# Kernel optimization log

Hardware: AMD Instinct MI355X
Metric: run time of the kernel (lower is better)

Reference implementation:

```python
import jax, jax.numpy as jnp
import numpy as np

B, N, E = 4, 20000, 320000          # batch, billboards, edges
F_NODE, F_AD = 16, 8                # raw feature dims
H, L, HEADS = 64, 2, 4              # hidden, message-passing layers, attn heads


def layer_norm(x, g, b, eps=1e-5):
    mu = x.mean(-1, keepdims=True)
    var = ((x - mu) ** 2).mean(-1, keepdims=True)
    return (x - mu) / jnp.sqrt(var + eps) * g + b


def setup_inputs() -> dict:
    key = jax.random.key(0)
    ks = jax.random.split(key, 16)
    s = lambda i, shape, sc: jax.random.normal(ks[i], shape, jnp.float32) * sc
    return {
        'graph_nodes': s(0, (B, N, F_NODE), 1.0),
        'current_ad': s(1, (B, F_AD), 1.0),
        'w_node': s(2, (F_NODE, H), 0.1), 'b_node': jnp.zeros((H,), jnp.float32),
        'msg_w': s(3, (L, 2 * H, H), 0.05), 'msg_b': jnp.zeros((L, H), jnp.float32),
        'upd_w': s(4, (L, 2 * H, H), 0.05), 'upd_b': jnp.zeros((L, H), jnp.float32),
        'w_ad': s(5, (F_AD, H), 0.1), 'b_ad': jnp.zeros((H,), jnp.float32),
        'wq': s(6, (H, H), 0.1), 'bq': jnp.zeros((H,), jnp.float32),
        'wk': s(7, (H, H), 0.1), 'bk': jnp.zeros((H,), jnp.float32),
        'wv': s(8, (H, H), 0.1), 'bv': jnp.zeros((H,), jnp.float32),
        'wo': s(9, (H, H), 0.1), 'bo': jnp.zeros((H,), jnp.float32),
        'ln_g': jnp.ones((H,), jnp.float32), 'ln_b': jnp.zeros((H,), jnp.float32),
        'policy_w': s(10, (H,), 0.1), 'policy_b': jnp.zeros((), jnp.float32),
        'graph_edge_links': jax.random.randint(ks[11], (B, 2, E), 0, N),
        'mask': jax.random.randint(ks[12], (B, N), 0, 2).astype(bool),
    }


def reference(graph_nodes, current_ad, w_node, b_node, msg_w, msg_b, upd_w, upd_b,
              w_ad, b_ad, wq, bq, wk, bk, wv, bv, wo, bo, ln_g, ln_b,
              policy_w, policy_b, graph_edge_links, mask):
    # ---- node encoder ----
    h = jax.nn.relu(graph_nodes @ w_node + b_node)          # [B,N,H]
    src = graph_edge_links[:, 0, :]                          # [B,E]
    dst = graph_edge_links[:, 1, :]                          # [B,E]
    gather = jax.vmap(lambda hh, ii: hh[ii])                 # per-batch edge gather
    scatter = jax.vmap(lambda m, d: jax.ops.segment_sum(m, d, num_segments=N))
    # ---- message passing: gather -> MLP message -> scatter-add -> residual update ----
    for l in range(L):
        edge_in = jnp.concatenate([gather(h, src), gather(h, dst)], axis=-1)  # [B,E,2H]
        msg = jax.nn.relu(edge_in @ msg_w[l] + msg_b[l])                       # [B,E,H]
        agg = scatter(msg, dst)                                                # [B,N,H]
        h = h + jax.nn.relu(jnp.concatenate([h, agg], axis=-1) @ upd_w[l] + upd_b[l])
    # ---- ad encoder + multi-head attention (query=ad, key/value=billboards) ----
    a = jax.nn.relu(current_ad @ w_ad + b_ad)                # [B,H]
    dh = H // HEADS
    q = (a @ wq + bq).reshape(B, HEADS, 1, dh)               # [B,h,1,d]
    k = (h @ wk + bk).reshape(B, N, HEADS, dh).transpose(0, 2, 1, 3)  # [B,h,N,d]
    v = (h @ wv + bv).reshape(B, N, HEADS, dh).transpose(0, 2, 1, 3)
    att = jax.nn.softmax(jnp.einsum('bhqd,bhkd->bhqk', q, k) / jnp.sqrt(jnp.float32(dh)), axis=-1)
    ctx = jnp.einsum('bhqk,bhkd->bhqd', att, v).reshape(B, H)
    g = layer_norm(a + ctx @ wo + bo, ln_g, ln_b)            # residual + LN, [B,H]
    # ---- masked policy logits over billboards ----
    logits = jnp.einsum('bnh,bh->bn', h, g) / jnp.sqrt(jnp.float32(H)) + h @ policy_w + policy_b
    return jnp.where(mask, logits, jnp.float32(-1e9))
```

## Files before the change

### kernel.cpp

```cpp
#include <hip/hip_runtime.h>
#include <hip/hip_bf16.h>
#include <math.h>

constexpr int B_ = 4;
constexpr int N_ = 20000;
constexpr int E_ = 320000;
constexpr int HEADS_ = 4;
constexpr int NCH = 64;
constexpr int CS = (N_ + NCH - 1) / NCH;
constexpr int NT_ = (B_ * N_) / 16;
constexpr int NWIN = 1250;
constexpr int HWIN = 625;
constexpr int WCAP = 512;
constexpr int TPAD = 16;

typedef __attribute__((ext_vector_type(8))) short short8;
typedef __attribute__((ext_vector_type(4))) float f32x4;

constexpr size_t SZ_TDB   = (size_t)B_ * N_ * 64 * 2;
constexpr size_t SZ_AGG   = (size_t)B_ * N_ * 64 * 4;
constexpr size_t SZ_EBUCK = (size_t)B_ * NWIN * WCAP * 4;
constexpr size_t SZ_EPAIR = (size_t)B_ * E_ * 4;
constexpr size_t OFF_TDB  = 0;
constexpr size_t OFF_AGG  = SZ_TDB;
constexpr size_t OFF_EBUCK= OFF_AGG + SZ_AGG;
constexpr size_t OFF_EPAIR= OFF_EBUCK + SZ_EBUCK;
constexpr size_t OFF_HB16 = OFF_EPAIR + SZ_EPAIR;
constexpr size_t OFF_AVEC = OFF_HB16 + SZ_TDB;
constexpr size_t OFF_Q    = OFF_AVEC + 1024;
constexpr size_t OFF_CTX  = OFF_Q + 1024;
constexpr size_t OFF_WCMB = OFF_CTX + 1024;
constexpr size_t OFF_FLAG = OFF_WCMB + 1024;
constexpr size_t OFF_PART = OFF_FLAG + 64;
constexpr size_t OFF_TAILS= OFF_PART + 1024 * 18 * 4 + 64;
constexpr size_t OFF_WBASE= OFF_TAILS + (size_t)B_ * NWIN * TPAD * 4;
constexpr size_t OFF_VB16 = OFF_WBASE + (size_t)B_ * NWIN * 4 + 64;

static __device__ __forceinline__ unsigned short f2bf(float f) {
    union { float f; unsigned u; } v; v.f = f;
    unsigned r = v.u + 0x7fffu + ((v.u >> 16) & 1u);
    return (unsigned short)(r >> 16);
}
static __device__ __forceinline__ float bf2f(unsigned short u) {
    union { unsigned u; float f; } v; v.u = (unsigned)u << 16;
    return v.f;
}

__global__ void k_maskdetect(const unsigned int* __restrict__ m, int* __restrict__ flag) {
    if (blockIdx.x == 0 && threadIdx.x == 0) {
        bool alli = true, allf = true;
        for (int i = 0; i < 256; ++i) {
            unsigned v = m[i];
            alli = alli && (v <= 1u);
            allf = allf && (v == 0u || v == 0x3f800000u);
        }
        *flag = alli ? 1 : (allf ? 2 : 0);
    }
}

__global__ __launch_bounds__(256) void k_embed_bucket(const float* __restrict__ gn,
                                                      const float* __restrict__ wnod,
                                                      const float* __restrict__ bias,
                                                      unsigned short* __restrict__ hb16,
                                                      const int* __restrict__ links,
                                                      int* __restrict__ tails,
                                                      unsigned* __restrict__ ebuck) {
    int i = blockIdx.x;
    int g = i >> 3, r = i & 7;
    if (g % 5 == 4) {
        int eb = (g / 5) * 8 + r;
        int lane = threadIdx.x & 63;
        float wc[16];
#pragma unroll
        for (int k = 0; k < 16; ++k) wc[k] = wnod[k * 64 + lane];
        float bb = bias[lane];
        int gw = eb * 4 + (threadIdx.x >> 6);
        for (int node = gw; node < B_ * N_; node += 1248 * 4) {
            const float* rr = gn + (size_t)node * 16;
            float a0 = 0.f, a1 = 0.f, a2 = 0.f, a3 = 0.f;
#pragma unroll
            for (int k = 0; k < 16; k += 4) {
                a0 = fmaf(rr[k + 0], wc[k + 0], a0);
                a1 = fmaf(rr[k + 1], wc[k + 1], a1);
                a2 = fmaf(rr[k + 2], wc[k + 2], a2);
                a3 = fmaf(rr[k + 3], wc[k + 3], a3);
            }
            float v = fmaxf(bb + ((a0 + a1) + (a2 + a3)), 0.f);
            hb16[(size_t)node * 64 + lane] = f2bf(v);
        }
    } else {
        int og = g - (g + 1) / 5;
        int b = r >> 1;
        int half = r & 1;
        int e0 = og * 512 + threadIdx.x;
        const int* lsrc = links + (size_t)b * 2 * E_;
#pragma unroll
        for (int ch = 0; ch < 2; ++ch) {
            int e = e0 + ch * 256;
            unsigned src = (unsigned)lsrc[e];
            unsigned dst = (unsigned)lsrc[E_ + e];
            int w = dst >> 4;
            if ((w >= HWIN) == (half == 1)) {
                int slot = atomicAdd(&tails[(b * NWIN + w) * TPAD], 1);
                if (slot < WCAP)
                    ebuck[(size_t)(b * NWIN + w) * WCAP + slot] = (dst << 16) | src;
            }
        }
    }
}

__global__ __launch_bounds__(1024) void k_scan_tails(const int* __restrict__ tails,
                                                     int* __restrict__ wbase) {
    __shared__ int wsum[16];
    __shared__ int sbase;
    int b = blockIdx.x, t = threadIdx.x;
    int lane = t & 63, wv = t >> 6;
    if (t == 0) sbase = 0;
    __syncthreads();
    for (int base = 0; base < NWIN; base += 1024) {
        int idx = base + t;
        int c = 0;
        if (idx < NWIN) { c = tails[(b * NWIN + idx) * TPAD]; if (c > WCAP) c = WCAP; }
        int x = c;
#pragma unroll
        for (int o = 1; o < 64; o <<= 1) {
            int y = __shfl_up(x, o);
            if (lane >= o) x += y;
        }
        if (lane == 63) wsum[wv] = x;
        __syncthreads();
        if (wv == 0) {
            int s = (lane < 16) ? wsum[lane] : 0;
#pragma unroll
            for (int o = 1; o < 16; o <<= 1) {
                int y = __shfl_up(s, o);
                if (lane >= o) s += y;
            }
            if (lane < 16) wsum[lane] = s;
        }
        __syncthreads();
        int wpre = (wv > 0) ? wsum[wv - 1] : 0;
        int incl = x + wpre + sbase;
        if (idx < NWIN) wbase[b * NWIN + idx] = incl - c;
        __syncthreads();
        if (t == 1023) sbase = incl;
        __syncthreads();
    }
}

__global__ __launch_bounds__(256) void k_sortwin(const unsigned* __restrict__ ebuck,
                                                 const int* __restrict__ tails,
                                                 const int* __restrict__ wbase,
                                                 unsigned* __restrict__ epair) {
    __shared__ int hist[16], hbase[16];
    __shared__ unsigned sbuf[WCAP];
    int i = blockIdx.x;
    int r = i & 7;
    int b = r >> 1;
    int w = (i >> 3) + HWIN * (r & 1);
    int cntw = tails[(b * NWIN + w) * TPAD];
    if (cntw > WCAP) cntw = WCAP;
    if (threadIdx.x < 16) hist[threadIdx.x] = 0;
    __syncthreads();
    const unsigned* src = ebuck + (size_t)(b * NWIN + w) * WCAP;
    int idx0 = threadIdx.x, idx1 = threadIdx.x + 256;
    bool v0 = idx0 < cntw, v1 = idx1 < cntw;
    unsigned e0 = 0, e1 = 0;
    if (v0) { e0 = src[idx0]; atomicAdd(&hist[(e0 >> 16) & 15], 1); }
    if (v1) { e1 = src[idx1]; atomicAdd(&hist[(e1 >> 16) & 15], 1); }
    __syncthreads();
    if (threadIdx.x == 0) {
        int run = 0;
#pragma unroll
        for (int p = 0; p < 16; ++p) { hbase[p] = run; run += hist[p]; }
    }
    __syncthreads();
    if (threadIdx.x < 16) hist[threadIdx.x] = 0;
    __syncthreads();
    if (v0) { int bn = (e0 >> 16) & 15; sbuf[hbase[bn] + atomicAdd(&hist[bn], 1)] = e0; }
    if (v1) { int bn = (e1 >> 16) & 15; sbuf[hbase[bn] + atomicAdd(&hist[bn], 1)] = e1; }
    __syncthreads();
    int gb = wbase[b * NWIN + w];
    unsigned* dst = epair + (size_t)b * E_ + gb;
    for (int idx = threadIdx.x; idx < cntw; idx += 256) dst[idx] = sbuf[idx];
}

__global__ __launch_bounds__(256) void k_tdst_mfma(const unsigned short* __restrict__ hb16,
                                                   const float* __restrict__ mw,
                                                   const float* __restrict__ mb,
                                                   unsigned short* __restrict__ tdb) {
    int lane = threadIdx.x & 63;
    int g = lane >> 4, c = lane & 15;
    short8 bf[4][2];
#pragma unroll
    for (int nt = 0; nt < 4; ++nt)
#pragma unroll
        for (int ks = 0; ks < 2; ++ks)
#pragma unroll
            for (int j = 0; j < 8; ++j)
                bf[nt][ks][j] = (short)f2bf(mw[(64 + ks * 32 + g * 8 + j) * 64 + nt * 16 + c]);
    float mbv[4];
#pragma unroll
    for (int nt = 0; nt < 4; ++nt) mbv[nt] = mb[nt * 16 + c];

    int wid = blockIdx.x * 4 + (threadIdx.x >> 6);
    int nw = gridDim.x * 4;
    f32x4 zero = {0.f, 0.f, 0.f, 0.f};
    for (int t = wid; t < NT_; t += nw) {
        const unsigned short* ap = hb16 + ((size_t)t * 16 + c) * 64;
        short8 a0 = *(const short8*)(ap + g * 8);
        short8 a1 = *(const short8*)(ap + 32 + g * 8);
        f32x4 acc[4];
#pragma unroll
        for (int nt = 0; nt < 4; ++nt) {
            acc[nt] = __builtin_amdgcn_mfma_f32_16x16x32_bf16(a0, bf[nt][0], zero, 0, 0, 0);
            acc[nt] = __builtin_amdgcn_mfma_f32_16x16x32_bf16(a1, bf[nt][1], acc[nt], 0, 0, 0);
        }
#pragma unroll
        for (int r = 0; r < 4; ++r) {
            size_t row = (size_t)t * 16 + 4 * g + r;
#pragma unroll
            for (int nt = 0; nt < 4; ++nt)
                tdb[row * 64 + nt * 16 + c] = f2bf(acc[nt][r] + mbv[nt]);
        }
    }
}

__global__ __launch_bounds__(256) void k_edge_mfma(const unsigned short* __restrict__ hb16,
                                                   const unsigned short* __restrict__ tdb,
                                                   const unsigned* __restrict__ epair,
                                                   const float* __restrict__ mw,
                                                   float* __restrict__ agg) {
    int lane = threadIdx.x & 63;
    int g = lane >> 4, c = lane & 15;
    short8 bf[4][2];
#pragma unroll
    for (int nt = 0; nt < 4; ++nt)
#pragma unroll
        for (int ks = 0; ks < 2; ++ks)
#pragma unroll
            for (int j = 0; j < 8; ++j)
                bf[nt][ks][j] = (short)f2bf(mw[(ks * 32 + g * 8 + j) * 64 + nt * 16 + c]);

    int i = blockIdx.x;
    int b = (i & 7) >> 1;
    int o = ((i >> 3) << 1) | (i & 1);
    int w = threadIdx.x >> 6;
    const unsigned* pp = epair + (size_t)b * E_;
    const unsigned short* hbase = hb16 + (size_t)(b * N_) * 64;
    const unsigned short* tbase = tdb + (size_t)(b * N_) * 64;
    float* abase = agg + (size_t)(b * N_) * 64;

    bool hi1 = (lane & 32) != 0;
    bool hi0 = (lane & 16) != 0;

    unsigned pr[4];
#pragma unroll
    for (int k = 0; k < 4; ++k) {
        int t0 = (o * 4 + w) + k * 5000;
        pr[k] = pp[t0 * 16 + c];
    }
    short8 a0[4], a1[4];
#pragma unroll
    for (int k = 0; k < 4; ++k) {
        const unsigned short* hrow = hbase + (size_t)(pr[k] & 0xFFFFu) * 64;
        a0[k] = *(const short8*)(hrow + g * 8);
        a1[k] = *(const short8*)(hrow + 32 + g * 8);
    }

    f32x4 zero = {0.f, 0.f, 0.f, 0.f};
#pragma unroll
    for (int k = 0; k < 4; ++k) {
        int dval = (int)(pr[k] >> 16);
        f32x4 acc[4];
#pragma unroll
        for (int nt = 0; nt < 4; ++nt) {
            acc[nt] = __builtin_amdgcn_mfma_f32_16x16x32_bf16(a0[k], bf[nt][0], zero, 0, 0, 0);
            acc[nt] = __builtin_amdgcn_mfma_f32_16x16x32_bf16(a1[k], bf[nt][1], acc[nt], 0, 0, 0);
        }

        int prev = __shfl(dval, (lane + 63) & 63);
        bool head = (c == 0) || (dval != prev);
        unsigned long long bal = __ballot(head);
        unsigned m16 = (unsigned)(bal & 0xFFFFu);

        while (m16) {
            int ii = __ffs(m16) - 1;
            unsigned rest = m16 & (m16 - 1);
            int jj = rest ? (__ffs(rest) - 1) : 16;
            m16 = rest;
            int d = __shfl(dval, ii);

            const unsigned short* trow = tbase + (size_t)d * 64;
            float t0v = bf2f(trow[c]);
            float t1v = bf2f(trow[16 + c]);
            float t2v = bf2f(trow[32 + c]);
            float t3v = bf2f(trow[48 + c]);

            float v0 = 0.f, v1 = 0.f, v2 = 0.f, v3 = 0.f;
#pragma unroll
            for (int r = 0; r < 4; ++r) {
                int rr = 4 * g + r;
                bool in = (rr >= ii) && (rr < jj);
                v0 += in ? fmaxf(acc[0][r] + t0v, 0.f) : 0.f;
                v1 += in ? fmaxf(acc[1][r] + t1v, 0.f) : 0.f;
                v2 += in ? fmaxf(acc[2][r] + t2v, 0.f) : 0.f;
                v3 += in ? fmaxf(acc[3][r] + t3v, 0.f) : 0.f;
            }
            float sA0 = hi1 ? v0 : v2;
            float sA1 = hi1 ? v1 : v3;
            float rA0 = __shfl_xor(sA0, 32);
            float rA1 = __shfl_xor(sA1, 32);
            float w0 = (hi1 ? v2 : v0) + rA0;
            float w1 = (hi1 ? v3 : v1) + rA1;
            float sB = hi0 ? w0 : w1;
            float rB = __shfl_xor(sB, 16);
            float outv = (hi0 ? w1 : w0) + rB;

            atomicAdd(&abase[(size_t)d * 64 + lane], outv);
        }
    }
}

__global__ __launch_bounds__(256) void k_upd_tdst_mfma(unsigned short* __restrict__ hb16,
                                                       const float* __restrict__ agg,
                                                       const float* __restrict__ uw,
                                                       const float* __restrict__ ub,
                                                       const float* __restrict__ mw2,
                                                       const float* __restrict__ mb2,
                                                       unsigned short* __restrict__ tdb) {
    __shared__ unsigned short stile[4][1024];
    int lane = threadIdx.x & 63;
    int g = lane >> 4, c = lane & 15;
    int wv = threadIdx.x >> 6;
    short8 bh[4][2], ba[4][2], bt[4][2];
#pragma unroll
    for (int nt = 0; nt < 4; ++nt)
#pragma unroll
        for (int ks = 0; ks < 2; ++ks)
#pragma unroll
            for (int j = 0; j < 8; ++j) {
                bh[nt][ks][j] = (short)f2bf(uw[(ks * 32 + g * 8 + j) * 64 + nt * 16 + c]);
                ba[nt][ks][j] = (short)f2bf(uw[(64 + ks * 32 + g * 8 + j) * 64 + nt * 16 + c]);
                bt[nt][ks][j] = (short)f2bf(mw2[(64 + ks * 32 + g * 8 + j) * 64 + nt * 16 + c]);
            }
    float ubv[4], mbv[4];
#pragma unroll
    for (int nt = 0; nt < 4; ++nt) { ubv[nt] = ub[nt * 16 + c]; mbv[nt] = mb2[nt * 16 + c]; }

    int wid = blockIdx.x * 4 + wv;
    int nw = gridDim.x * 4;
    f32x4 zero = {0.f, 0.f, 0.f, 0.f};
    int xr = (c & 7) << 3;
    for (int t = wid; t < NT_; t += nw) {
        unsigned short* ap = hb16 + ((size_t)t * 16 + c) * 64;
        short8 a0 = *(const short8*)(ap + g * 8);
        short8 a1 = *(const short8*)(ap + 32 + g * 8);

        const float* gp = agg + ((size_t)t * 16 + c) * 64;
        float4 q0 = *(const float4*)(gp + g * 8);
        float4 q1 = *(const float4*)(gp + g * 8 + 4);
        float4 q2 = *(const float4*)(gp + 32 + g * 8);
        float4 q3 = *(const float4*)(gp + 32 + g * 8 + 4);
        short8 s0, s1;
        s0[0] = (short)f2bf(q0.x); s0[1] = (short)f2bf(q0.y);
        s0[2] = (short)f2bf(q0.z); s0[3] = (short)f2bf(q0.w);
        s0[4] = (short)f2bf(q1.x); s0[5] = (short)f2bf(q1.y);
        s0[6] = (short)f2bf(q1.z); s0[7] = (short)f2bf(q1.w);
        s1[0] = (short)f2bf(q2.x); s1[1] = (short)f2bf(q2.y);
        s1[2] = (short)f2bf(q2.z); s1[3] = (short)f2bf(q2.w);
        s1[4] = (short)f2bf(q3.x); s1[5] = (short)f2bf(q3.y);
        s1[6] = (short)f2bf(q3.z); s1[7] = (short)f2bf(q3.w);

        f32x4 acc[4];
#pragma unroll
        for (int nt = 0; nt < 4; ++nt) {
            acc[nt] = __builtin_amdgcn_mfma_f32_16x16x32_bf16(a0, bh[nt][0], zero, 0, 0, 0);
            acc[nt] = __builtin_amdgcn_mfma_f32_16x16x32_bf16(a1, bh[nt][1], acc[nt], 0, 0, 0);
            acc[nt] = __builtin_amdgcn_mfma_f32_16x16x32_bf16(s0, ba[nt][0], acc[nt], 0, 0, 0);
            acc[nt] = __builtin_amdgcn_mfma_f32_16x16x32_bf16(s1, ba[nt][1], acc[nt], 0, 0, 0);
        }
#pragma unroll
        for (int r = 0; r < 4; ++r) {
            size_t row = (size_t)t * 16 + 4 * g + r;
            int lrow = 4 * g + r;
#pragma unroll
            for (int nt = 0; nt < 4; ++nt) {
                size_t idx = row * 64 + nt * 16 + c;
                float v = bf2f(hb16[idx]) + fmaxf(acc[nt][r] + ubv[nt], 0.f);
                unsigned short vb = f2bf(v);
                hb16[idx] = vb;
                int col = nt * 16 + c;
                stile[wv][lrow * 64 + (col ^ ((lrow & 7) << 3))] = vb;
            }
        }
        short8 na0 = *(const short8*)&stile[wv][c * 64 + ((g * 8) ^ xr)];
        short8 na1 = *(const short8*)&stile[wv][c * 64 + ((32 + g * 8) ^ xr)];
        f32x4 tacc[4];
#pragma unroll
        for (int nt = 0; nt < 4; ++nt) {
            tacc[nt] = __builtin_amdgcn_mfma_f32_16x16x32_bf16(na0, bt[nt][0], zero, 0, 0, 0);
            tacc[nt] = __builtin_amdgcn_mfma_f32_16x16x32_bf16(na1, bt[nt][1], tacc[nt], 0, 0, 0);
        }
#pragma unroll
        for (int r = 0; r < 4; ++r) {
            size_t row = (size_t)t * 16 + 4 * g + r;
#pragma unroll
            for (int nt = 0; nt < 4; ++nt)
                tdb[row * 64 + nt * 16 + c] = f2bf(tacc[nt][r] + mbv[nt]);
        }
    }
}

__global__ __launch_bounds__(256) void k_upd_kv_mfma(unsigned short* __restrict__ hb16,
                                                     const float* __restrict__ agg,
                                                     const float* __restrict__ uw,
                                                     const float* __restrict__ ub,
                                                     const float* __restrict__ wk,
                                                     const float* __restrict__ bk,
                                                     const float* __restrict__ wv,
                                                     const float* __restrict__ bv,
                                                     unsigned short* __restrict__ kb16,
                                                     unsigned short* __restrict__ vb16) {
    __shared__ unsigned short stile[4][1024];
    int lane = threadIdx.x & 63;
    int g = lane >> 4, c = lane & 15;
    int wvv = threadIdx.x >> 6;
    short8 bh[4][2], ba[4][2], bkf[4][2], bvf[4][2];
#pragma unroll
    for (int nt = 0; nt < 4; ++nt)
#pragma unroll
        for (int ks = 0; ks < 2; ++ks)
#pragma unroll
            for (int j = 0; j < 8; ++j) {
                bh[nt][ks][j]  = (short)f2bf(uw[(ks * 32 + g * 8 + j) * 64 + nt * 16 + c]);
                ba[nt][ks][j]  = (short)f2bf(uw[(64 + ks * 32 + g * 8 + j) * 64 + nt * 16 + c]);
                bkf[nt][ks][j] = (short)f2bf(wk[(ks * 32 + g * 8 + j) * 64 + nt * 16 + c]);
                bvf[nt][ks][j] = (short)f2bf(wv[(ks * 32 + g * 8 + j) * 64 + nt * 16 + c]);
            }
    float ubv[4], bkv[4], bvv[4];
#pragma unroll
    for (int nt = 0; nt < 4; ++nt) {
        ubv[nt] = ub[nt * 16 + c];
        bkv[nt] = bk[nt * 16 + c];
        bvv[nt] = bv[nt * 16 + c];
    }

    int wid = blockIdx.x * 4 + wvv;
    int nw = gridDim.x * 4;
    f32x4 zero = {0.f, 0.f, 0.f, 0.f};
    int xr = (c & 7) << 3;
    for (int t = wid; t < NT_; t += nw) {
        unsigned short* ap = hb16 + ((size_t)t * 16 + c) * 64;
        short8 a0 = *(const short8*)(ap + g * 8);
        short8 a1 = *(const short8*)(ap + 32 + g * 8);

        const float* gp = agg + ((size_t)t * 16 + c) * 64;
        float4 q0 = *(const float4*)(gp + g * 8);
        float4 q1 = *(const float4*)(gp + g * 8 + 4);
        float4 q2 = *(const float4*)(gp + 32 + g * 8);
        float4 q3 = *(const float4*)(gp + 32 + g * 8 + 4);
        short8 s0, s1;
        s0[0] = (short)f2bf(q0.x); s0[1] = (short)f2bf(q0.y);
        s0[2] = (short)f2bf(q0.z); s0[3] = (short)f2bf(q0.w);
        s0[4] = (short)f2bf(q1.x); s0[5] = (short)f2bf(q1.y);
        s0[6] = (short)f2bf(q1.z); s0[7] = (short)f2bf(q1.w);
        s1[0] = (short)f2bf(q2.x); s1[1] = (short)f2bf(q2.y);
        s1[2] = (short)f2bf(q2.z); s1[3] = (short)f2bf(q2.w);
        s1[4] = (short)f2bf(q3.x); s1[5] = (short)f2bf(q3.y);
        s1[6] = (short)f2bf(q3.z); s1[7] = (short)f2bf(q3.w);

        f32x4 acc[4];
#pragma unroll
        for (int nt = 0; nt < 4; ++nt) {
            acc[nt] = __builtin_amdgcn_mfma_f32_16x16x32_bf16(a0, bh[nt][0], zero, 0, 0, 0);
            acc[nt] = __builtin_amdgcn_mfma_f32_16x16x32_bf16(a1, bh[nt][1], acc[nt], 0, 0, 0);
            acc[nt] = __builtin_amdgcn_mfma_f32_16x16x32_bf16(s0, ba[nt][0], acc[nt], 0, 0, 0);
            acc[nt] = __builtin_amdgcn_mfma_f32_16x16x32_bf16(s1, ba[nt][1], acc[nt], 0, 0, 0);
        }
#pragma unroll
        for (int r = 0; r < 4; ++r) {
            size_t row = (size_t)t * 16 + 4 * g + r;
            int lrow = 4 * g + r;
#pragma unroll
            for (int nt = 0; nt < 4; ++nt) {
                size_t idx = row * 64 + nt * 16 + c;
                float v = bf2f(hb16[idx]) + fmaxf(acc[nt][r] + ubv[nt], 0.f);
                unsigned short vb = f2bf(v);
                hb16[idx] = vb;
                int col = nt * 16 + c;
                stile[wvv][lrow * 64 + (col ^ ((lrow & 7) << 3))] = vb;
            }
        }
        short8 na0 = *(const short8*)&stile[wvv][c * 64 + ((g * 8) ^ xr)];
        short8 na1 = *(const short8*)&stile[wvv][c * 64 + ((32 + g * 8) ^ xr)];
        f32x4 ak[4], av[4];
#pragma unroll
        for (int nt = 0; nt < 4; ++nt) {
            ak[nt] = __builtin_amdgcn_mfma_f32_16x16x32_bf16(na0, bkf[nt][0], zero, 0, 0, 0);
            ak[nt] = __builtin_amdgcn_mfma_f32_16x16x32_bf16(na1, bkf[nt][1], ak[nt], 0, 0, 0);
            av[nt] = __builtin_amdgcn_mfma_f32_16x16x32_bf16(na0, bvf[nt][0], zero, 0, 0, 0);
            av[nt] = __builtin_amdgcn_mfma_f32_16x16x32_bf16(na1, bvf[nt][1], av[nt], 0, 0, 0);
        }
#pragma unroll
        for (int r = 0; r < 4; ++r) {
            size_t row = (size_t)t * 16 + 4 * g + r;
#pragma unroll
            for (int nt = 0; nt < 4; ++nt) {
                kb16[row * 64 + nt * 16 + c] = f2bf(ak[nt][r] + bkv[nt]);
                vb16[row * 64 + nt * 16 + c] = f2bf(av[nt][r] + bvv[nt]);
            }
        }
    }
}

__global__ __launch_bounds__(64) void k_aq(const float* __restrict__ ad,
                                           const float* __restrict__ wad,
                                           const float* __restrict__ bad,
                                           const float* __restrict__ wq,
                                           const float* __restrict__ bq,
                                           float* __restrict__ a_out,
                                           float* __restrict__ q_out) {
    int b = blockIdx.x, t = threadIdx.x;
    __shared__ float sa[64];
    float acc = bad[t];
#pragma unroll
    for (int i = 0; i < 8; ++i) acc = fmaf(ad[b * 8 + i], wad[i * 64 + t], acc);
    float av = fmaxf(acc, 0.f);
    sa[t] = av;
    a_out[b * 64 + t] = av;
    __syncthreads();
    float qa = bq[t];
    for (int i = 0; i < 64; ++i) qa = fmaf(sa[i], wq[i * 64 + t], qa);
    q_out[b * 64 + t] = qa;
}

__global__ __launch_bounds__(256) void k_attn(const float* __restrict__ q,
                                              const unsigned short* __restrict__ kb16,
                                              const unsigned short* __restrict__ vb16,
                                              float* __restrict__ part) {
    int id = blockIdx.x;
    int ch = id % NCH;
    int bh = id / NCH;
    int b = bh / HEADS_, hd = bh % HEADS_;
    float qv[16];
#pragma unroll
    for (int d = 0; d < 16; ++d) qv[d] = q[b * 64 + hd * 16 + d];
    float m = -1e30f, s = 0.f, c[16];
#pragma unroll
    for (int d = 0; d < 16; ++d) c[d] = 0.f;
    int n0 = ch * CS;
    int n1 = n0 + CS; if (n1 > N_) n1 = N_;
    for (int n = n0 + threadIdx.x; n < n1; n += 256) {
        const short8* kr = (const short8*)(kb16 + ((size_t)b * N_ + n) * 64 + hd * 16);
        short8 k0 = kr[0], k1 = kr[1];
        float dot = 0.f;
#pragma unroll
        for (int d = 0; d < 8; ++d) {
            dot = fmaf(qv[d], bf2f((unsigned short)k0[d]), dot);
            dot = fmaf(qv[8 + d], bf2f((unsigned short)k1[d]), dot);
        }
        dot *= 0.25f;
        float nm = fmaxf(m, dot);
        float p = __expf(dot - nm);
        float cor = __expf(m - nm);
        const short8* vr = (const short8*)(vb16 + ((size_t)b * N_ + n) * 64 + hd * 16);
        short8 v0 = vr[0], v1 = vr[1];
        s = s * cor + p;
#pragma unroll
        for (int d = 0; d < 8; ++d) {
            c[d] = c[d] * cor + p * bf2f((unsigned short)v0[d]);
            c[8 + d] = c[8 + d] * cor + p * bf2f((unsigned short)v1[d]);
        }
        m = nm;
    }
#pragma unroll
    for (int o = 1; o < 64; o <<= 1) {
        float m2 = __shfl_xor(m, o);
        float s2 = __shfl_xor(s, o);
        float nm = fmaxf(m, m2);
        float w1 = __expf(m - nm), w2 = __expf(m2 - nm);
        s = s * w1 + s2 * w2;
#pragma unroll
        for (int d = 0; d < 16; ++d) {
            float c2 = __shfl_xor(c[d], o);
            c[d] = c[d] * w1 + c2 * w2;
        }
        m = nm;
    }
    __shared__ float red[4][18];
    int wv_ = threadIdx.x >> 6, lane = threadIdx.x & 63;
    if (lane == 0) {
        red[wv_][0] = m; red[wv_][1] = s;
#pragma unroll
        for (int d = 0; d < 16; ++d) red[wv_][2 + d] = c[d];
    }
    __syncthreads();
    if (threadIdx.x == 0) {
        float gm = red[0][0];
        for (int w = 1; w < 4; ++w) gm = fmaxf(gm, red[w][0]);
        float gs = 0.f, gc[16];
#pragma unroll
        for (int d = 0; d < 16; ++d) gc[d] = 0.f;
        for (int w = 0; w < 4; ++w) {
            float ww = __expf(red[w][0] - gm);
            gs += red[w][1] * ww;
#pragma unroll
            for (int d = 0; d < 16; ++d) gc[d] += red[w][2 + d] * ww;
        }
        float* p = part + (size_t)id * 18;
        p[0] = gm; p[1] = gs;
#pragma unroll
        for (int d = 0; d < 16; ++d) p[2 + d] = gc[d];
    }
}

__global__ __launch_bounds__(64) void k_comb(const float* __restrict__ part,
                                             float* __restrict__ ctx) {
    int bh = blockIdx.x, t = threadIdx.x;
    int b = bh / HEADS_, hd = bh % HEADS_;
    const float* p = part + ((size_t)bh * NCH + t) * 18;
    float m = p[0], s = p[1], c[16];
#pragma unroll
    for (int d = 0; d < 16; ++d) c[d] = p[2 + d];
    float gm = m;
#pragma unroll
    for (int o = 1; o < 64; o <<= 1) gm = fmaxf(gm, __shfl_xor(gm, o));
    float w = __expf(m - gm);
    float sw = s * w;
#pragma unroll
    for (int o = 1; o < 64; o <<= 1) sw += __shfl_xor(sw, o);
    float cg[16];
#pragma unroll
    for (int d = 0; d < 16; ++d) {
        float x = c[d] * w;
#pragma unroll
        for (int o = 1; o < 64; o <<= 1) x += __shfl_xor(x, o);
        cg[d] = x;
    }
    if (t == 0) {
#pragma unroll
        for (int d = 0; d < 16; ++d) ctx[b * 64 + hd * 16 + d] = cg[d] / sw;
    }
}

__global__ __launch_bounds__(64) void k_g(const float* __restrict__ a,
                                          const float* __restrict__ ctx,
                                          const float* __restrict__ wo,
                                          const float* __restrict__ bo,
                                          const float* __restrict__ lng,
                                          const float* __restrict__ lnb,
                                          const float* __restrict__ pw,
                                          float* __restrict__ wcomb) {
    int b = blockIdx.x, t = threadIdx.x;
    __shared__ float sc[64];
    sc[t] = ctx[b * 64 + t];
    __syncthreads();
    float o = bo[t];
    for (int i = 0; i < 64; ++i) o = fmaf(sc[i], wo[i * 64 + t], o);
    float y = a[b * 64 + t] + o;
    float mu = y;
#pragma unroll
    for (int oo = 1; oo < 64; oo <<= 1) mu += __shfl_xor(mu, oo);
    mu *= (1.f / 64.f);
    float d = y - mu;
    float var = d * d;
#pragma unroll
    for (int oo = 1; oo < 64; oo <<= 1) var += __shfl_xor(var, oo);
    var *= (1.f / 64.f);
    float g = d * rsqrtf(var + 1e-5f) * lng[t] + lnb[t];
    wcomb[b * 64 + t] = g * 0.125f + pw[t];
}

__global__ __launch_bounds__(256) void k_final(const unsigned short* __restrict__ hb16,
                                               const float* __restrict__ wcomb,
                                               const float* __restrict__ pb,
                                               const void* __restrict__ mask,
                                               const int* __restrict__ flagp,
                                               float* __restrict__ out) {
    int idx = blockIdx.x * 256 + threadIdx.x;
    if (idx >= B_ * N_) return;
    int b = idx / N_;
    const float* wr = wcomb + b * 64;
    const short8* hr = (const short8*)(hb16 + (size_t)idx * 64);
    float acc = pb[0];
#pragma unroll
    for (int i = 0; i < 8; ++i) {
        short8 hv = hr[i];
#pragma unroll
        for (int j = 0; j < 8; ++j)
            acc = fmaf(bf2f((unsigned short)hv[j]), wr[i * 8 + j], acc);
    }
    int flag = *flagp;
    bool mv;
    if (flag == 1)      mv = ((const int*)mask)[idx] != 0;
    else if (flag == 2) mv = ((const float*)mask)[idx] != 0.f;
    else                mv = ((const unsigned char*)mask)[idx] != 0;
    out[idx] = mv ? acc : -1.0e9f;
}

extern "C" void kernel_launch(void* const* d_in, const int* in_sizes, int n_in,
                              void* d_out, int out_size, void* d_ws, size_t ws_size,
                              hipStream_t stream) {
    const float* gn   = (const float*)d_in[0];
    const float* ad   = (const float*)d_in[1];
    const float* wnod = (const float*)d_in[2];
    const float* bnod = (const float*)d_in[3];
    const float* msgw = (const float*)d_in[4];
    const float* msgb = (const float*)d_in[5];
    const float* updw = (const float*)d_in[6];
    const float* updb = (const float*)d_in[7];
    const float* wad  = (const float*)d_in[8];
    const float* bad  = (const float*)d_in[9];
    const float* wq   = (const float*)d_in[10];
    const float* bq   = (const float*)d_in[11];
    const float* wk   = (const float*)d_in[12];
    const float* bk   = (const float*)d_in[13];
    const float* wv   = (const float*)d_in[14];
    const float* bv   = (const float*)d_in[15];
    const float* wo   = (const float*)d_in[16];
    const float* bo   = (const float*)d_in[17];
    const float* lng  = (const float*)d_in[18];
    const float* lnb  = (const float*)d_in[19];
    const float* pw   = (const float*)d_in[20];
    const float* pb   = (const float*)d_in[21];
    const int*   links= (const int*)d_in[22];
    const void*  mask = d_in[23];

    char* ws = (char*)d_ws;
    unsigned short* tdb  = (unsigned short*)(ws + OFF_TDB);
    unsigned short* kb16 = (unsigned short*)(ws + OFF_TDB);
    float* agg  = (float*)(ws + OFF_AGG);
    unsigned* ebuck = (unsigned*)(ws + OFF_EBUCK);
    unsigned* epair = (unsigned*)(ws + OFF_EPAIR);
    unsigned short* hb16 = (unsigned short*)(ws + OFF_HB16);
    float* avec = (float*)(ws + OFF_AVEC);
    float* qvec = (float*)(ws + OFF_Q);
    float* ctx  = (float*)(ws + OFF_CTX);
    float* wcmb = (float*)(ws + OFF_WCMB);
    int*   flag = (int*)(ws + OFF_FLAG);
    float* part = (float*)(ws + OFF_PART);
    int*   tails= (int*)(ws + OFF_TAILS);
    int*   wbase= (int*)(ws + OFF_WBASE);
    unsigned short* vb16 = (unsigned short*)(ws + OFF_VB16);
    float* out  = (float*)d_out;

    hipMemsetAsync(tails, 0, (size_t)B_ * NWIN * TPAD * 4, stream);
    k_maskdetect<<<1, 1, 0, stream>>>((const unsigned int*)mask, flag);
    k_embed_bucket<<<6248, 256, 0, stream>>>(gn, wnod, bnod, hb16, links, tails, ebuck);
    k_scan_tails<<<B_, 1024, 0, stream>>>(tails, wbase);
    k_sortwin<<<5000, 256, 0, stream>>>(ebuck, tails, wbase, epair);

    k_tdst_mfma<<<512, 256, 0, stream>>>(hb16, msgw, msgb, tdb);
    hipMemsetAsync(agg, 0, SZ_AGG, stream);
    k_edge_mfma<<<5000, 256, 0, stream>>>(hb16, tdb, epair, msgw, agg);
    k_upd_tdst_mfma<<<512, 256, 0, stream>>>(hb16, agg, updw, updb,
                                             msgw + (size_t)128 * 64, msgb + 64, tdb);
    hipMemsetAsync(agg, 0, SZ_AGG, stream);
    k_edge_mfma<<<5000, 256, 0, stream>>>(hb16, tdb, epair, msgw + (size_t)128 * 64, agg);
    k_upd_kv_mfma<<<512, 256, 0, stream>>>(hb16, agg, updw + (size_t)128 * 64, updb + 64,
                                           wk, bk, wv, bv, kb16, vb16);

    k_aq<<<B_, 64, 0, stream>>>(ad, wad, bad, wq, bq, avec, qvec);
    k_attn<<<B_ * HEADS_ * NCH, 256, 0, stream>>>(qvec, kb16, vb16, part);
    k_comb<<<B_ * HEADS_, 64, 0, stream>>>(part, ctx);
    k_g<<<B_, 64, 0, stream>>>(avec, ctx, wo, bo, lng, lnb, pw, wcmb);
    k_final<<<(B_ * N_ + 255) / 256, 256, 0, stream>>>(hb16, wcmb, pb, mask, flag, out);
}
```

Before: 272.1 us.

## Interleave tdst bf16 layout and load per-edge dst terms once before segment loop

The tdst buffer now stores a row in an interleaved column order, so each lane writes and reads its four columns (c, 16+c, 32+c, 48+c) as one 64-bit access instead of four scattered 16-bit ones. The edge kernel now loads each edge row's dst term and applies bias+ReLU once before the segmented reduction loop. Previously it reloaded the dst row for every destination segment. This cuts the number of memory transactions and repeated work in the hot edge kernel. In exchange it adds four shuffles per edge tile, and every reader of tdb must use the new interleaved layout.

```diff
diff --git a/kernel.cpp b/kernel.cpp
--- a/kernel.cpp
+++ b/kernel.cpp
@@ -219,9 +219,12 @@
 #pragma unroll
         for (int r = 0; r < 4; ++r) {
             size_t row = (size_t)t * 16 + 4 * g + r;
-#pragma unroll
-            for (int nt = 0; nt < 4; ++nt)
-                tdb[row * 64 + nt * 16 + c] = f2bf(acc[nt][r] + mbv[nt]);
+            unsigned long long pk =
+                (unsigned long long)f2bf(acc[0][r] + mbv[0])
+              | ((unsigned long long)f2bf(acc[1][r] + mbv[1]) << 16)
+              | ((unsigned long long)f2bf(acc[2][r] + mbv[2]) << 32)
+              | ((unsigned long long)f2bf(acc[3][r] + mbv[3]) << 48);
+            *(unsigned long long*)(tdb + row * 64 + c * 4) = pk;
         }
     }
 }
@@ -279,6 +282,17 @@
             acc[nt] = __builtin_amdgcn_mfma_f32_16x16x32_bf16(a1[k], bf[nt][1], acc[nt], 0, 0, 0);
         }
 
+        float val[4][4];
+#pragma unroll
+        for (int r = 0; r < 4; ++r) {
+            int dr = __shfl(dval, 4 * g + r);
+            unsigned long long tv = *(const unsigned long long*)(tbase + (size_t)dr * 64 + c * 4);
+            val[0][r] = fmaxf(acc[0][r] + bf2f((unsigned short)(tv       & 0xFFFFu)), 0.f);
+            val[1][r] = fmaxf(acc[1][r] + bf2f((unsigned short)((tv >> 16) & 0xFFFFu)), 0.f);
+            val[2][r] = fmaxf(acc[2][r] + bf2f((unsigned short)((tv >> 32) & 0xFFFFu)), 0.f);
+            val[3][r] = fmaxf(acc[3][r] + bf2f((unsigned short)((tv >> 48) & 0xFFFFu)), 0.f);
+        }
+
         int prev = __shfl(dval, (lane + 63) & 63);
         bool head = (c == 0) || (dval != prev);
         unsigned long long bal = __ballot(head);
@@ -291,21 +305,15 @@
             m16 = rest;
             int d = __shfl(dval, ii);
 
-            const unsigned short* trow = tbase + (size_t)d * 64;
-            float t0v = bf2f(trow[c]);
-            float t1v = bf2f(trow[16 + c]);
-            float t2v = bf2f(trow[32 + c]);
-            float t3v = bf2f(trow[48 + c]);
-
             float v0 = 0.f, v1 = 0.f, v2 = 0.f, v3 = 0.f;
 #pragma unroll
             for (int r = 0; r < 4; ++r) {
                 int rr = 4 * g + r;
                 bool in = (rr >= ii) && (rr < jj);
-                v0 += in ? fmaxf(acc[0][r] + t0v, 0.f) : 0.f;
-                v1 += in ? fmaxf(acc[1][r] + t1v, 0.f) : 0.f;
-                v2 += in ? fmaxf(acc[2][r] + t2v, 0.f) : 0.f;
-                v3 += in ? fmaxf(acc[3][r] + t3v, 0.f) : 0.f;
+                v0 += in ? val[0][r] : 0.f;
+                v1 += in ? val[1][r] : 0.f;
+                v2 += in ? val[2][r] : 0.f;
+                v3 += in ? val[3][r] : 0.f;
             }
             float sA0 = hi1 ? v0 : v2;
             float sA1 = hi1 ? v1 : v3;
@@ -405,9 +413,12 @@
 #pragma unroll
         for (int r = 0; r < 4; ++r) {
             size_t row = (size_t)t * 16 + 4 * g + r;
-#pragma unroll
-            for (int nt = 0; nt < 4; ++nt)
-                tdb[row * 64 + nt * 16 + c] = f2bf(tacc[nt][r] + mbv[nt]);
+            unsigned long long pk =
+                (unsigned long long)f2bf(tacc[0][r] + mbv[0])
+              | ((unsigned long long)f2bf(tacc[1][r] + mbv[1]) << 16)
+              | ((unsigned long long)f2bf(tacc[2][r] + mbv[2]) << 32)
+              | ((unsigned long long)f2bf(tacc[3][r] + mbv[3]) << 48);
+            *(unsigned long long*)(tdb + row * 64 + c * 4) = pk;
         }
     }
 }
```

Result: faster. 257.1 us (-5.5%).
